# Kernel optimization log

Hardware: AMD Instinct MI355X
Metric: run time of the kernel (lower is better)

The kernel has to match this reference:

```python
import jax, jax.numpy as jnp
import numpy as np

N = 100_000      # nodes
F_IN = 128       # in_channels
C = 128          # out_channels
H = 2 * C        # conv1 output dim
E = 1_000_000    # edges per graph
EPS = 1e-12      # F.normalize eps


def setup_inputs() -> dict:
    key = jax.random.key(0)
    k = jax.random.split(key, 5)
    x = jax.random.normal(k[0], (N, F_IN), jnp.float32)
    edge_index_top = jax.random.randint(k[1], (2, E), 0, N, dtype=jnp.int64)
    edge_index_last = jax.random.randint(k[2], (2, E), 0, N, dtype=jnp.int64)
    W1 = jax.random.normal(k[3], (F_IN, H), jnp.float32) / np.sqrt(F_IN)
    b1 = jnp.zeros((H,), jnp.float32)
    return {"x": x, "edge_index_top": edge_index_top,
            "edge_index_last": edge_index_last, "W1": W1, "b1": b1}


def gcn_conv(x, W, b, src, dst, n):
    """PyG GCNConv: out = D^{-1/2} (A + I) D^{-1/2} X W + b, deg over A+I."""
    xw = x @ W                                           # [N, H]
    ones = jnp.ones(src.shape[0], xw.dtype)
    deg = jax.ops.segment_sum(ones, dst, num_segments=n) + 1.0  # +1 self loop
    dinv = jax.lax.rsqrt(deg)                            # [N]
    norm = dinv[src] * dinv[dst]                         # [E]
    agg = jax.ops.segment_sum(norm[:, None] * xw[src], dst, num_segments=n)
    agg = agg + (dinv * dinv)[:, None] * xw              # self-loop term
    return agg + b


def reference(x, edge_index_top, edge_index_last, W1, b1):
    n = x.shape[0]
    # F.normalize(x, dim=1)
    xn = x / jnp.clip(jnp.linalg.norm(x, axis=1, keepdims=True), EPS)
    src_t, dst_t = edge_index_top[0], edge_index_top[1]
    ztop = gcn_conv(xn, W1, b1, src_t, dst_t, n)         # [N, H]
    # aedge = sigmoid(ztop @ ztop.T)[src, dst] without materializing NxN
    aedge = jax.nn.sigmoid(jnp.sum(ztop[src_t] * ztop[dst_t], axis=-1))  # [E]
    zlast = gcn_conv(xn, W1, b1, edge_index_last[0], edge_index_last[1], n)
    return (ztop, zlast, aedge)
```

## Files before the change

### kernel.cpp

```cpp
#include <hip/hip_runtime.h>
#include <hip/hip_bf16.h>

typedef __bf16 bf16_t;
typedef __bf16 bf16x4 __attribute__((ext_vector_type(4)));
typedef __bf16 bf16x8 __attribute__((ext_vector_type(8)));
typedef float  f32x4  __attribute__((ext_vector_type(4)));

#define N_NODES 100000
#define F_INC   128
#define HDIM    256
#define NEDGE   1000000
#define ELL_CAP 48
#define GATHER_BLKS (N_NODES / 4)
#define GEMM_BLKS   ((N_NODES / 16 + 3) / 4)
#define FILL_BLKS   ((NEDGE + 255) / 256)

__global__ void zero_cnt(int* __restrict__ cnt, int n) {
    int i = blockIdx.x * 256 + threadIdx.x;
    if (i < n) cnt[i] = 0;
}

__global__ void detect_kernel(const int* __restrict__ eit, const int* __restrict__ eil,
                              int* __restrict__ flags) {
    int lane = threadIdx.x & 63;
    const int* p = (threadIdx.x < 64) ? eit : eil;
    int s = (p[2 * lane + 1] != 0) ? 1 : 0;
    #pragma unroll
    for (int off = 1; off < 64; off <<= 1) s += __shfl_xor(s, off, 64);
    if (lane == 0) flags[(threadIdx.x < 64) ? 0 : 1] = (s == 0) ? 1 : 0;
}

__global__ void wprep_kernel(const float* __restrict__ W1, bf16_t* __restrict__ wlay,
                             bf16_t* __restrict__ xw, bf16_t* __restrict__ zb) {
    int t = blockIdx.x * 256 + threadIdx.x;
    if (blockIdx.x == 0) {
        xw[(size_t)N_NODES * HDIM + threadIdx.x] = (bf16_t)0.f;
        zb[(size_t)N_NODES * HDIM + threadIdx.x] = (bf16_t)0.f;
    }
    int j = t & 7, lane = (t >> 3) & 63, kk = (t >> 9) & 3, nt = t >> 11;
    int m = lane & 15, q = lane >> 4;
    int k = kk * 32 + q * 8 + j;
    int n = nt * 16 + m;
    wlay[t] = (bf16_t)W1[k * HDIM + n];
}

__device__ __forceinline__ void gemm_body(int w, int lane, const float* __restrict__ x,
                                          const bf16_t* __restrict__ wlay,
                                          bf16_t* __restrict__ xw) {
    if (w >= N_NODES / 16) return;
    int m = lane & 15, q = lane >> 4;
    int r0 = w * 16;
    int row = r0 + m;
    const float4* xr = (const float4*)(x + (size_t)row * F_INC);
    float4 u[8];
    #pragma unroll
    for (int kk = 0; kk < 4; kk++) {
        u[2 * kk]     = xr[kk * 8 + q * 2];
        u[2 * kk + 1] = xr[kk * 8 + q * 2 + 1];
    }
    float ss = 0.f;
    #pragma unroll
    for (int j = 0; j < 8; j++)
        ss += u[j].x * u[j].x + u[j].y * u[j].y + u[j].z * u[j].z + u[j].w * u[j].w;
    ss += __shfl_xor(ss, 16, 64);
    ss += __shfl_xor(ss, 32, 64);
    float rv = 1.0f / fmaxf(sqrtf(ss), 1e-12f);
    bf16x8 a[4];
    #pragma unroll
    for (int kk = 0; kk < 4; kk++) {
        float4 p0 = u[2 * kk], p1 = u[2 * kk + 1];
        a[kk][0] = (bf16_t)(p0.x * rv); a[kk][1] = (bf16_t)(p0.y * rv);
        a[kk][2] = (bf16_t)(p0.z * rv); a[kk][3] = (bf16_t)(p0.w * rv);
        a[kk][4] = (bf16_t)(p1.x * rv); a[kk][5] = (bf16_t)(p1.y * rv);
        a[kk][6] = (bf16_t)(p1.z * rv); a[kk][7] = (bf16_t)(p1.w * rv);
    }
    const bf16x8* wl = (const bf16x8*)wlay;
    #pragma unroll
    for (int nt = 0; nt < 16; nt++) {
        f32x4 c = {0.f, 0.f, 0.f, 0.f};
        c = __builtin_amdgcn_mfma_f32_16x16x32_bf16(a[0], wl[(nt * 4 + 0) * 64 + lane], c, 0, 0, 0);
        c = __builtin_amdgcn_mfma_f32_16x16x32_bf16(a[1], wl[(nt * 4 + 1) * 64 + lane], c, 0, 0, 0);
        c = __builtin_amdgcn_mfma_f32_16x16x32_bf16(a[2], wl[(nt * 4 + 2) * 64 + lane], c, 0, 0, 0);
        c = __builtin_amdgcn_mfma_f32_16x16x32_bf16(a[3], wl[(nt * 4 + 3) * 64 + lane], c, 0, 0, 0);
        #pragma unroll
        for (int i = 0; i < 4; i++) {
            xw[(size_t)(r0 + q * 4 + i) * HDIM + nt * 16 + m] = (bf16_t)c[i];
        }
    }
}

__device__ __forceinline__ void fill2_body(int e, const int* __restrict__ ei,
                                           const int* __restrict__ flag,
                                           int* __restrict__ cnt, int* __restrict__ ell2) {
    if (e >= NEDGE) return;
    int f = *flag;
    int src = ei[e << f];
    int dst = ei[(NEDGE + e) << f];
    int slot = atomicAdd(&cnt[dst], 1);
    if (slot < ELL_CAP) {
        int2 pr; pr.x = src; pr.y = e;
        ((int2*)ell2)[(size_t)dst * ELL_CAP + slot] = pr;
    }
}

__device__ __forceinline__ void fill_body(int e, const int* __restrict__ ei,
                                          const int* __restrict__ flag,
                                          int* __restrict__ cnt, int* __restrict__ ell) {
    if (e >= NEDGE) return;
    int f = *flag;
    int src = ei[e << f];
    int dst = ei[(NEDGE + e) << f];
    int slot = atomicAdd(&cnt[dst], 1);
    if (slot < ELL_CAP) ell[dst * ELL_CAP + slot] = src;
}

__global__ __launch_bounds__(256) void gemm_fill_kernel(const float* __restrict__ x,
                                                        const bf16_t* __restrict__ wlay,
                                                        bf16_t* __restrict__ xw,
                                                        const int* __restrict__ ei,
                                                        const int* __restrict__ flag,
                                                        int* __restrict__ cnt,
                                                        int* __restrict__ ell2) {
    if (blockIdx.x < GEMM_BLKS) {
        gemm_body(blockIdx.x * 4 + (threadIdx.x >> 6), threadIdx.x & 63, x, wlay, xw);
    } else {
        fill2_body((blockIdx.x - GEMM_BLKS) * 256 + threadIdx.x, ei, flag, cnt, ell2);
    }
}

__global__ void dinvpad_kernel(const int* __restrict__ cnt, float* __restrict__ dinv,
                               int* __restrict__ ell, int paired) {
    int i = blockIdx.x * 256 + threadIdx.x;
    if (i >= N_NODES) {
        if (i == N_NODES) dinv[N_NODES] = 0.f;
        return;
    }
    int c = cnt[i];
    dinv[i] = rsqrtf((float)c + 1.0f);
    int deg = (c > ELL_CAP) ? ELL_CAP : c;
    int r4 = (deg + 3) & ~3;
    if (paired) {
        int2 pr; pr.x = N_NODES; pr.y = -1;
        for (int s = deg; s < r4; s++) ((int2*)ell)[(size_t)i * ELL_CAP + s] = pr;
    } else {
        for (int s = deg; s < r4; s++) ell[i * ELL_CAP + s] = N_NODES;
    }
}

template<bool PAIRED>
__device__ __forceinline__ void gather_body(int i, int lane, const int* __restrict__ ell,
                                            const int* __restrict__ cnt,
                                            const float* __restrict__ dinv,
                                            const bf16_t* __restrict__ xw,
                                            const float* __restrict__ b1,
                                            float* __restrict__ out,
                                            bf16_t* __restrict__ zb) {
    float di = dinv[i];
    const bf16x4* xws = (const bf16x4*)xw;
    bf16x4 sv = xws[(size_t)i * 64 + lane];
    float acc0 = di * (float)sv.x;
    float acc1 = di * (float)sv.y;
    float acc2 = di * (float)sv.z;
    float acc3 = di * (float)sv.w;
    int deg = cnt[i];
    if (deg > ELL_CAP) deg = ELL_CAP;
    int nit = (deg + 3) >> 2;
    int4 sa, sb;
    if (PAIRED) {
        const int4* e8 = (const int4*)ell + (size_t)i * (ELL_CAP / 2);
        sa = e8[0]; sb = e8[1];
        for (int b = 0; b < nit; b++) {
            int bn = (b + 1 < nit) ? (b + 1) : b;
            int4 na = e8[2 * bn], nb = e8[2 * bn + 1];
            int s0 = sa.x, s1 = sa.z, s2 = sb.x, s3 = sb.z;
            float d0 = dinv[s0], d1 = dinv[s1], d2 = dinv[s2], d3 = dinv[s3];
            bf16x4 v0 = xws[(size_t)s0 * 64 + lane];
            bf16x4 v1 = xws[(size_t)s1 * 64 + lane];
            bf16x4 v2 = xws[(size_t)s2 * 64 + lane];
            bf16x4 v3 = xws[(size_t)s3 * 64 + lane];
            acc0 += d0 * (float)v0.x + d1 * (float)v1.x + d2 * (float)v2.x + d3 * (float)v3.x;
            acc1 += d0 * (float)v0.y + d1 * (float)v1.y + d2 * (float)v2.y + d3 * (float)v3.y;
            acc2 += d0 * (float)v0.z + d1 * (float)v1.z + d2 * (float)v2.z + d3 * (float)v3.z;
            acc3 += d0 * (float)v0.w + d1 * (float)v1.w + d2 * (float)v2.w + d3 * (float)v3.w;
            sa = na; sb = nb;
        }
    } else {
        const int4* el4 = (const int4*)(ell + (size_t)i * ELL_CAP);
        sa = el4[0];
        for (int b = 0; b < nit; b++) {
            int bn = (b + 1 < nit) ? (b + 1) : b;
            int4 na = el4[bn];
            int s0 = sa.x, s1 = sa.y, s2 = sa.z, s3 = sa.w;
            float d0 = dinv[s0], d1 = dinv[s1], d2 = dinv[s2], d3 = dinv[s3];
            bf16x4 v0 = xws[(size_t)s0 * 64 + lane];
            bf16x4 v1 = xws[(size_t)s1 * 64 + lane];
            bf16x4 v2 = xws[(size_t)s2 * 64 + lane];
            bf16x4 v3 = xws[(size_t)s3 * 64 + lane];
            acc0 += d0 * (float)v0.x + d1 * (float)v1.x + d2 * (float)v2.x + d3 * (float)v3.x;
            acc1 += d0 * (float)v0.y + d1 * (float)v1.y + d2 * (float)v2.y + d3 * (float)v3.y;
            acc2 += d0 * (float)v0.z + d1 * (float)v1.z + d2 * (float)v2.z + d3 * (float)v3.z;
            acc3 += d0 * (float)v0.w + d1 * (float)v1.w + d2 * (float)v2.w + d3 * (float)v3.w;
            sa = na;
        }
    }
    float4 bv = ((const float4*)b1)[lane];
    f32x4 o;
    o[0] = di * acc0 + bv.x;
    o[1] = di * acc1 + bv.y;
    o[2] = di * acc2 + bv.z;
    o[3] = di * acc3 + bv.w;
    __builtin_nontemporal_store(o, (f32x4*)out + (size_t)i * 64 + lane);
    if (zb) {
        bf16x4 zo;
        zo.x = (bf16_t)o[0]; zo.y = (bf16_t)o[1]; zo.z = (bf16_t)o[2]; zo.w = (bf16_t)o[3];
        ((bf16x4*)zb)[(size_t)i * 64 + lane] = zo;
    }
}

__global__ __launch_bounds__(256) void gather_fill_kernel(const int* __restrict__ ell2,
                                                          const int* __restrict__ cnt,
                                                          const float* __restrict__ dinv,
                                                          const bf16_t* __restrict__ xw,
                                                          const float* __restrict__ b1,
                                                          float* __restrict__ out,
                                                          bf16_t* __restrict__ zb,
                                                          const int* __restrict__ ei_l,
                                                          const int* __restrict__ flag_l,
                                                          int* __restrict__ cnt_l,
                                                          int* __restrict__ ell_l) {
    if (blockIdx.x < FILL_BLKS) {
        fill_body(blockIdx.x * 256 + threadIdx.x, ei_l, flag_l, cnt_l, ell_l);
    } else {
        gather_body<true>((blockIdx.x - FILL_BLKS) * 4 + (threadIdx.x >> 6), threadIdx.x & 63,
                          ell2, cnt, dinv, xw, b1, out, zb);
    }
}

__device__ __forceinline__ void aedge_dst_body(int i, int lane, const int* __restrict__ ell2,
                                               const int* __restrict__ cnt,
                                               const bf16_t* __restrict__ zb,
                                               float* __restrict__ aedge) {
    int sub = lane & 15, g = lane >> 4;
    const bf16x8* z8 = (const bf16x8*)zb;
    bf16x8 d0 = z8[(size_t)i * 32 + sub * 2];
    bf16x8 d1 = z8[(size_t)i * 32 + sub * 2 + 1];
    int deg = cnt[i];
    if (deg > ELL_CAP) deg = ELL_CAP;
    int nit = (deg + 3) >> 2;
    if (nit == 0) return;
    const int2* pr = (const int2*)ell2 + (size_t)i * ELL_CAP;
    int2 pe = pr[g];
    for (int b = 0; b < nit; b++) {
        int bn = (b + 1 < nit) ? (b + 1) : b;
        int2 pn = pr[bn * 4 + g];
        int src = pe.x, eid = pe.y;
        bf16x8 a0 = z8[(size_t)src * 32 + sub * 2];
        bf16x8 a1 = z8[(size_t)src * 32 + sub * 2 + 1];
        float p = 0.f;
        #pragma unroll
        for (int j = 0; j < 8; j++)
            p += (float)a0[j] * (float)d0[j] + (float)a1[j] * (float)d1[j];
        #pragma unroll
        for (int off = 1; off < 16; off <<= 1) p += __shfl_xor(p, off, 64);
        if (sub == 0 && eid >= 0)
            __builtin_nontemporal_store(1.0f / (1.0f + __expf(-p)), &aedge[eid]);
        pe = pn;
    }
}

__global__ __launch_bounds__(256) void fused_last_kernel(const int* __restrict__ ell_l,
                                                         const int* __restrict__ cnt_l,
                                                         const float* __restrict__ dinv_l,
                                                         const bf16_t* __restrict__ xw,
                                                         const float* __restrict__ b1,
                                                         float* __restrict__ out1,
                                                         const int* __restrict__ ell2_t,
                                                         const int* __restrict__ cnt_t,
                                                         const bf16_t* __restrict__ zb,
                                                         float* __restrict__ aedge) {
    int lane = threadIdx.x & 63;
    int node = (blockIdx.x >> 1) * 4 + (threadIdx.x >> 6);
    if (blockIdx.x & 1) {
        aedge_dst_body(node, lane, ell2_t, cnt_t, zb, aedge);
    } else {
        gather_body<false>(node, lane, ell_l, cnt_l, dinv_l, xw, b1, out1, (bf16_t*)0);
    }
}

extern "C" void kernel_launch(void* const* d_in, const int* in_sizes, int n_in,
                              void* d_out, int out_size, void* d_ws, size_t ws_size,
                              hipStream_t stream) {
    const float* x       = (const float*)d_in[0];
    const int*   ei_top  = (const int*)d_in[1];
    const int*   ei_last = (const int*)d_in[2];
    const float* W1      = (const float*)d_in[3];
    const float* b1      = (const float*)d_in[4];
    float* out = (float*)d_out;

    char* ws = (char*)d_ws;
    bf16_t* xw     = (bf16_t*)(ws);
    bf16_t* zb     = (bf16_t*)(ws + 51201024);
    int*    ell2t  = (int*)  (ws + 102402048);
    int*    ell_l  = (int*)  (ws + 140802048);
    float*  dinv_t = (float*)(ws + 160002048);
    float*  dinv_l = (float*)(ws + 160402112);
    int*    cnt_t  = (int*)  (ws + 160802176);
    int*    cnt_l  = (int*)  (ws + 161202176);
    bf16_t* wlay   = (bf16_t*)(ws + 161602176);
    int*    flags  = (int*)  (ws + 161667712);

    zero_cnt<<<(2 * N_NODES + 255) / 256, 256, 0, stream>>>(cnt_t, 2 * N_NODES);
    detect_kernel<<<1, 128, 0, stream>>>(ei_top, ei_last, flags);
    wprep_kernel<<<128, 256, 0, stream>>>(W1, wlay, xw, zb);
    gemm_fill_kernel<<<GEMM_BLKS + FILL_BLKS, 256, 0, stream>>>(x, wlay, xw,
                                                                ei_top, flags, cnt_t, ell2t);
    dinvpad_kernel<<<(N_NODES + 256) / 256 + 1, 256, 0, stream>>>(cnt_t, dinv_t, ell2t, 1);
    gather_fill_kernel<<<FILL_BLKS + GATHER_BLKS, 256, 0, stream>>>(
        ell2t, cnt_t, dinv_t, xw, b1, out, zb, ei_last, flags + 1, cnt_l, ell_l);
    dinvpad_kernel<<<(N_NODES + 256) / 256 + 1, 256, 0, stream>>>(cnt_l, dinv_l, ell_l, 0);
    fused_last_kernel<<<2 * GATHER_BLKS, 256, 0, stream>>>(
        ell_l, cnt_l, dinv_l, xw, b1, out + (size_t)N_NODES * HDIM,
        ell2t, cnt_t, zb, out + (size_t)2 * N_NODES * HDIM);
}
```

Baseline: 637.9 us.

## Merge prep kernels and widen gather/aedge loops to 8 neighbors per iteration

Merges the zero-count, layout-detect and weight-prep kernels into one launch to cut launch overhead. The ELL neighbor loops in the gather and aedge bodies now handle 8 neighbors per iteration instead of 4. Index lists are read with nontemporal loads, replacing the software prefetch of the next index block. Padding is rounded to multiples of 8, which adds more padded dummy gathers for low-degree nodes in exchange for more loads in flight per wave.

```diff
diff --git a/kernel.cpp b/kernel.cpp
--- a/kernel.cpp
+++ b/kernel.cpp
@@ -5,6 +5,8 @@
 typedef __bf16 bf16x4 __attribute__((ext_vector_type(4)));
 typedef __bf16 bf16x8 __attribute__((ext_vector_type(8)));
 typedef float  f32x4  __attribute__((ext_vector_type(4)));
+typedef int    i32x2  __attribute__((ext_vector_type(2)));
+typedef int    i32x4  __attribute__((ext_vector_type(4)));
 
 #define N_NODES 100000
 #define F_INC   128
@@ -14,34 +16,42 @@
 #define GATHER_BLKS (N_NODES / 4)
 #define GEMM_BLKS   ((N_NODES / 16 + 3) / 4)
 #define FILL_BLKS   ((NEDGE + 255) / 256)
-
-__global__ void zero_cnt(int* __restrict__ cnt, int n) {
-    int i = blockIdx.x * 256 + threadIdx.x;
-    if (i < n) cnt[i] = 0;
-}
-
-__global__ void detect_kernel(const int* __restrict__ eit, const int* __restrict__ eil,
-                              int* __restrict__ flags) {
-    int lane = threadIdx.x & 63;
-    const int* p = (threadIdx.x < 64) ? eit : eil;
-    int s = (p[2 * lane + 1] != 0) ? 1 : 0;
-    #pragma unroll
-    for (int off = 1; off < 64; off <<= 1) s += __shfl_xor(s, off, 64);
-    if (lane == 0) flags[(threadIdx.x < 64) ? 0 : 1] = (s == 0) ? 1 : 0;
-}
-
-__global__ void wprep_kernel(const float* __restrict__ W1, bf16_t* __restrict__ wlay,
-                             bf16_t* __restrict__ xw, bf16_t* __restrict__ zb) {
-    int t = blockIdx.x * 256 + threadIdx.x;
-    if (blockIdx.x == 0) {
-        xw[(size_t)N_NODES * HDIM + threadIdx.x] = (bf16_t)0.f;
-        zb[(size_t)N_NODES * HDIM + threadIdx.x] = (bf16_t)0.f;
-    }
-    int j = t & 7, lane = (t >> 3) & 63, kk = (t >> 9) & 3, nt = t >> 11;
-    int m = lane & 15, q = lane >> 4;
-    int k = kk * 32 + q * 8 + j;
-    int n = nt * 16 + m;
-    wlay[t] = (bf16_t)W1[k * HDIM + n];
+#define ZERO_BLKS   ((2 * N_NODES + 255) / 256)
+
+__global__ __launch_bounds__(256) void prep_kernel(int* __restrict__ cnt,
+                                                   const int* __restrict__ eit,
+                                                   const int* __restrict__ eil,
+                                                   int* __restrict__ flags,
+                                                   const float* __restrict__ W1,
+                                                   bf16_t* __restrict__ wlay,
+                                                   bf16_t* __restrict__ xw,
+                                                   bf16_t* __restrict__ zb) {
+    int bid = blockIdx.x;
+    if (bid < ZERO_BLKS) {
+        int i = bid * 256 + threadIdx.x;
+        if (i < 2 * N_NODES) cnt[i] = 0;
+    } else if (bid == ZERO_BLKS) {
+        if (threadIdx.x < 128) {
+            int lane = threadIdx.x & 63;
+            const int* p = (threadIdx.x < 64) ? eit : eil;
+            int s = (p[2 * lane + 1] != 0) ? 1 : 0;
+            #pragma unroll
+            for (int off = 1; off < 64; off <<= 1) s += __shfl_xor(s, off, 64);
+            if (lane == 0) flags[(threadIdx.x < 64) ? 0 : 1] = (s == 0) ? 1 : 0;
+        }
+    } else {
+        int w = bid - ZERO_BLKS - 1;
+        int t = w * 256 + threadIdx.x;
+        if (w == 0) {
+            xw[(size_t)N_NODES * HDIM + threadIdx.x] = (bf16_t)0.f;
+            zb[(size_t)N_NODES * HDIM + threadIdx.x] = (bf16_t)0.f;
+        }
+        int j = t & 7, lane = (t >> 3) & 63, kk = (t >> 9) & 3, nt = t >> 11;
+        int m = lane & 15, q = lane >> 4;
+        int k = kk * 32 + q * 8 + j;
+        int n = nt * 16 + m;
+        wlay[t] = (bf16_t)W1[k * HDIM + n];
+    }
 }
 
 __device__ __forceinline__ void gemm_body(int w, int lane, const float* __restrict__ x,
@@ -138,12 +148,12 @@
     int c = cnt[i];
     dinv[i] = rsqrtf((float)c + 1.0f);
     int deg = (c > ELL_CAP) ? ELL_CAP : c;
-    int r4 = (deg + 3) & ~3;
+    int r8 = (deg + 7) & ~7;
     if (paired) {
         int2 pr; pr.x = N_NODES; pr.y = -1;
-        for (int s = deg; s < r4; s++) ((int2*)ell)[(size_t)i * ELL_CAP + s] = pr;
-    } else {
-        for (int s = deg; s < r4; s++) ell[i * ELL_CAP + s] = N_NODES;
+        for (int s = deg; s < r8; s++) ((int2*)ell)[(size_t)i * ELL_CAP + s] = pr;
+    } else {
+        for (int s = deg; s < r8; s++) ell[i * ELL_CAP + s] = N_NODES;
     }
 }
 
@@ -164,44 +174,42 @@
     float acc3 = di * (float)sv.w;
     int deg = cnt[i];
     if (deg > ELL_CAP) deg = ELL_CAP;
-    int nit = (deg + 3) >> 2;
-    int4 sa, sb;
-    if (PAIRED) {
-        const int4* e8 = (const int4*)ell + (size_t)i * (ELL_CAP / 2);
-        sa = e8[0]; sb = e8[1];
-        for (int b = 0; b < nit; b++) {
-            int bn = (b + 1 < nit) ? (b + 1) : b;
-            int4 na = e8[2 * bn], nb = e8[2 * bn + 1];
-            int s0 = sa.x, s1 = sa.z, s2 = sb.x, s3 = sb.z;
-            float d0 = dinv[s0], d1 = dinv[s1], d2 = dinv[s2], d3 = dinv[s3];
-            bf16x4 v0 = xws[(size_t)s0 * 64 + lane];
-            bf16x4 v1 = xws[(size_t)s1 * 64 + lane];
-            bf16x4 v2 = xws[(size_t)s2 * 64 + lane];
-            bf16x4 v3 = xws[(size_t)s3 * 64 + lane];
-            acc0 += d0 * (float)v0.x + d1 * (float)v1.x + d2 * (float)v2.x + d3 * (float)v3.x;
-            acc1 += d0 * (float)v0.y + d1 * (float)v1.y + d2 * (float)v2.y + d3 * (float)v3.y;
-            acc2 += d0 * (float)v0.z + d1 * (float)v1.z + d2 * (float)v2.z + d3 * (float)v3.z;
-            acc3 += d0 * (float)v0.w + d1 * (float)v1.w + d2 * (float)v2.w + d3 * (float)v3.w;
-            sa = na; sb = nb;
-        }
-    } else {
-        const int4* el4 = (const int4*)(ell + (size_t)i * ELL_CAP);
-        sa = el4[0];
-        for (int b = 0; b < nit; b++) {
-            int bn = (b + 1 < nit) ? (b + 1) : b;
-            int4 na = el4[bn];
-            int s0 = sa.x, s1 = sa.y, s2 = sa.z, s3 = sa.w;
-            float d0 = dinv[s0], d1 = dinv[s1], d2 = dinv[s2], d3 = dinv[s3];
-            bf16x4 v0 = xws[(size_t)s0 * 64 + lane];
-            bf16x4 v1 = xws[(size_t)s1 * 64 + lane];
-            bf16x4 v2 = xws[(size_t)s2 * 64 + lane];
-            bf16x4 v3 = xws[(size_t)s3 * 64 + lane];
-            acc0 += d0 * (float)v0.x + d1 * (float)v1.x + d2 * (float)v2.x + d3 * (float)v3.x;
-            acc1 += d0 * (float)v0.y + d1 * (float)v1.y + d2 * (float)v2.y + d3 * (float)v3.y;
-            acc2 += d0 * (float)v0.z + d1 * (float)v1.z + d2 * (float)v2.z + d3 * (float)v3.z;
-            acc3 += d0 * (float)v0.w + d1 * (float)v1.w + d2 * (float)v2.w + d3 * (float)v3.w;
-            sa = na;
-        }
+    int nit = (deg + 7) >> 3;
+    for (int b = 0; b < nit; b++) {
+        int s0, s1, s2, s3, s4, s5, s6, s7;
+        if (PAIRED) {
+            const i32x4* e8 = (const i32x4*)ell + (size_t)i * (ELL_CAP / 2) + 4 * b;
+            i32x4 A = __builtin_nontemporal_load(e8);
+            i32x4 B = __builtin_nontemporal_load(e8 + 1);
+            i32x4 C = __builtin_nontemporal_load(e8 + 2);
+            i32x4 D = __builtin_nontemporal_load(e8 + 3);
+            s0 = A[0]; s1 = A[2]; s2 = B[0]; s3 = B[2];
+            s4 = C[0]; s5 = C[2]; s6 = D[0]; s7 = D[2];
+        } else {
+            const i32x4* el4 = (const i32x4*)(ell + (size_t)i * ELL_CAP) + 2 * b;
+            i32x4 A = __builtin_nontemporal_load(el4);
+            i32x4 B = __builtin_nontemporal_load(el4 + 1);
+            s0 = A[0]; s1 = A[1]; s2 = A[2]; s3 = A[3];
+            s4 = B[0]; s5 = B[1]; s6 = B[2]; s7 = B[3];
+        }
+        bf16x4 v0 = xws[(size_t)s0 * 64 + lane];
+        bf16x4 v1 = xws[(size_t)s1 * 64 + lane];
+        bf16x4 v2 = xws[(size_t)s2 * 64 + lane];
+        bf16x4 v3 = xws[(size_t)s3 * 64 + lane];
+        bf16x4 v4 = xws[(size_t)s4 * 64 + lane];
+        bf16x4 v5 = xws[(size_t)s5 * 64 + lane];
+        bf16x4 v6 = xws[(size_t)s6 * 64 + lane];
+        bf16x4 v7 = xws[(size_t)s7 * 64 + lane];
+        float d0 = dinv[s0], d1 = dinv[s1], d2 = dinv[s2], d3 = dinv[s3];
+        float d4 = dinv[s4], d5 = dinv[s5], d6 = dinv[s6], d7 = dinv[s7];
+        acc0 += d0 * (float)v0.x + d1 * (float)v1.x + d2 * (float)v2.x + d3 * (float)v3.x
+              + d4 * (float)v4.x + d5 * (float)v5.x + d6 * (float)v6.x + d7 * (float)v7.x;
+        acc1 += d0 * (float)v0.y + d1 * (float)v1.y + d2 * (float)v2.y + d3 * (float)v3.y
+              + d4 * (float)v4.y + d5 * (float)v5.y + d6 * (float)v6.y + d7 * (float)v7.y;
+        acc2 += d0 * (float)v0.z + d1 * (float)v1.z + d2 * (float)v2.z + d3 * (float)v3.z
+              + d4 * (float)v4.z + d5 * (float)v5.z + d6 * (float)v6.z + d7 * (float)v7.z;
+        acc3 += d0 * (float)v0.w + d1 * (float)v1.w + d2 * (float)v2.w + d3 * (float)v3.w
+              + d4 * (float)v4.w + d5 * (float)v5.w + d6 * (float)v6.w + d7 * (float)v7.w;
     }
     float4 bv = ((const float4*)b1)[lane];
     f32x4 o;
@@ -236,35 +244,43 @@
     }
 }
 
-__device__ __forceinline__ void aedge_dst_body(int i, int lane, const int* __restrict__ ell2,
-                                               const int* __restrict__ cnt,
-                                               const bf16_t* __restrict__ zb,
-                                               float* __restrict__ aedge) {
+__device__ __forceinline__ void aedge_body(int i, int lane, const int* __restrict__ ell2,
+                                           const int* __restrict__ cnt,
+                                           const bf16_t* __restrict__ zb,
+                                           float* __restrict__ aedge) {
     int sub = lane & 15, g = lane >> 4;
     const bf16x8* z8 = (const bf16x8*)zb;
     bf16x8 d0 = z8[(size_t)i * 32 + sub * 2];
     bf16x8 d1 = z8[(size_t)i * 32 + sub * 2 + 1];
     int deg = cnt[i];
     if (deg > ELL_CAP) deg = ELL_CAP;
-    int nit = (deg + 3) >> 2;
-    if (nit == 0) return;
-    const int2* pr = (const int2*)ell2 + (size_t)i * ELL_CAP;
-    int2 pe = pr[g];
+    int nit = (deg + 7) >> 3;
+    const i32x2* pr = (const i32x2*)ell2 + (size_t)i * ELL_CAP;
     for (int b = 0; b < nit; b++) {
-        int bn = (b + 1 < nit) ? (b + 1) : b;
-        int2 pn = pr[bn * 4 + g];
-        int src = pe.x, eid = pe.y;
-        bf16x8 a0 = z8[(size_t)src * 32 + sub * 2];
-        bf16x8 a1 = z8[(size_t)src * 32 + sub * 2 + 1];
-        float p = 0.f;
+        i32x2 pA = __builtin_nontemporal_load(pr + b * 8 + g);
+        i32x2 pB = __builtin_nontemporal_load(pr + b * 8 + 4 + g);
+        int sA = pA[0], sB = pB[0];
+        bf16x8 a0 = z8[(size_t)sA * 32 + sub * 2];
+        bf16x8 a1 = z8[(size_t)sA * 32 + sub * 2 + 1];
+        bf16x8 c0 = z8[(size_t)sB * 32 + sub * 2];
+        bf16x8 c1 = z8[(size_t)sB * 32 + sub * 2 + 1];
+        float p = 0.f, q = 0.f;
         #pragma unroll
-        for (int j = 0; j < 8; j++)
+        for (int j = 0; j < 8; j++) {
             p += (float)a0[j] * (float)d0[j] + (float)a1[j] * (float)d1[j];
+            q += (float)c0[j] * (float)d0[j] + (float)c1[j] * (float)d1[j];
+        }
         #pragma unroll
-        for (int off = 1; off < 16; off <<= 1) p += __shfl_xor(p, off, 64);
-        if (sub == 0 && eid >= 0)
-            __builtin_nontemporal_store(1.0f / (1.0f + __expf(-p)), &aedge[eid]);
-        pe = pn;
+        for (int off = 1; off < 16; off <<= 1) {
+            p += __shfl_xor(p, off, 64);
+            q += __shfl_xor(q, off, 64);
+        }
+        if (sub == 0) {
+            if (pA[1] >= 0)
+                __builtin_nontemporal_store(1.0f / (1.0f + __expf(-p)), &aedge[pA[1]]);
+            if (pB[1] >= 0)
+                __builtin_nontemporal_store(1.0f / (1.0f + __expf(-q)), &aedge[pB[1]]);
+        }
     }
 }
 
@@ -281,7 +297,7 @@
     int lane = threadIdx.x & 63;
     int node = (blockIdx.x >> 1) * 4 + (threadIdx.x >> 6);
     if (blockIdx.x & 1) {
-        aedge_dst_body(node, lane, ell2_t, cnt_t, zb, aedge);
+        aedge_body(node, lane, ell2_t, cnt_t, zb, aedge);
     } else {
         gather_body<false>(node, lane, ell_l, cnt_l, dinv_l, xw, b1, out1, (bf16_t*)0);
     }
@@ -309,9 +325,8 @@
     bf16_t* wlay   = (bf16_t*)(ws + 161602176);
     int*    flags  = (int*)  (ws + 161667712);
 
-    zero_cnt<<<(2 * N_NODES + 255) / 256, 256, 0, stream>>>(cnt_t, 2 * N_NODES);
-    detect_kernel<<<1, 128, 0, stream>>>(ei_top, ei_last, flags);
-    wprep_kernel<<<128, 256, 0, stream>>>(W1, wlay, xw, zb);
+    prep_kernel<<<ZERO_BLKS + 1 + 128, 256, 0, stream>>>(cnt_t, ei_top, ei_last, flags,
+                                                         W1, wlay, xw, zb);
     gemm_fill_kernel<<<GEMM_BLKS + FILL_BLKS, 256, 0, stream>>>(x, wlay, xw,
                                                                 ei_top, flags, cnt_t, ell2t);
     dinvpad_kernel<<<(N_NODES + 256) / 256 + 1, 256, 0, stream>>>(cnt_t, dinv_t, ell2t, 1);
```

After: 677.6 us. 1.06x slower.
